# Kernel optimization log

Hardware: AMD Instinct MI355X
Metric: run time of the kernel (lower is better)

Reference implementation:

```python
import jax, jax.numpy as jnp
import numpy as np

B, D = 4096, 128
TEMPERATURE = 0.2

def setup_inputs() -> dict:
    key = jax.random.key(0)
    k1, k2 = jax.random.split(key)
    z1 = jax.random.normal(k1, (B, D), dtype=jnp.float32)
    z2 = jax.random.normal(k2, (B, D), dtype=jnp.float32)
    return {"z1": z1, "z2": z2}

def reference(z1, z2):
    # single-process path: global batch == local batch
    gb = z1.shape[0]
    z = jnp.concatenate([z1, z2], axis=0)              # [2B, D]
    sim = jnp.matmul(z, z.T) / TEMPERATURE             # [2B, 2B]
    n = 2 * gb
    diag = jnp.eye(n, dtype=bool)
    sim = jnp.where(diag, jnp.finfo(sim.dtype).min, sim)
    targets = jnp.concatenate([jnp.arange(gb, n), jnp.arange(0, gb)])
    logp = jax.nn.log_softmax(sim, axis=-1)            # [2B, 2B]
    loss_all = -logp[jnp.arange(n), targets]           # [2B]
    # rank 0, world_size 1 -> idx_keep covers all rows
    return loss_all.mean()
```

## Files before the change

kernel.cpp:

```cpp
#include <hip/hip_runtime.h>
#include <stdint.h>

typedef unsigned short u16;
typedef unsigned int u32;

#define NTOT 8192
#define BH   4096
#define DD   128
#define COLSPLIT 8
#define COLS_PER_SPLIT (NTOT / COLSPLIT)
#define TILE_COLS 128
#define TILES_PER_SPLIT (COLS_PER_SPLIT / TILE_COLS)
#define ROWS_PER_BLOCK 128
#define ROWS_PER_WAVE 32
#define LDS_PITCH 136
#define NEG_INF (-3.0e38f)
#define SCALE_IN 2.68579144f
#define LN2F 0.6931471805599453f

typedef __bf16 bf16x8 __attribute__((ext_vector_type(8)));
typedef float  f32x4  __attribute__((ext_vector_type(4)));

__device__ __forceinline__ u16 f2bf(float f) {
  u32 u = __float_as_uint(f);
  return (u16)((u + 0x7fffu + ((u >> 16) & 1u)) >> 16);
}

__device__ __forceinline__ float fexp2(float x) {
#if __has_builtin(__builtin_amdgcn_exp2f)
  return __builtin_amdgcn_exp2f(x);
#else
  float r; asm("v_exp_f32 %0, %1" : "=v"(r) : "v"(x)); return r;
#endif
}

__global__ __launch_bounds__(256) void ntx_convert(
    const float* __restrict__ z1, const float* __restrict__ z2,
    u16* __restrict__ zb, float* __restrict__ out) {
  if (blockIdx.x == 0 && threadIdx.x == 0) out[0] = 0.f;
  const int i = (blockIdx.x * 256 + threadIdx.x) * 4;
  const int half = BH * DD;
  float4 v = (i < half) ? *reinterpret_cast<const float4*>(z1 + i)
                        : *reinterpret_cast<const float4*>(z2 + (i - half));
  u32 lo = (u32)f2bf(v.x * SCALE_IN) | ((u32)f2bf(v.y * SCALE_IN) << 16);
  u32 hi = (u32)f2bf(v.z * SCALE_IN) | ((u32)f2bf(v.w * SCALE_IN) << 16);
  uint2 o; o.x = lo; o.y = hi;
  *reinterpret_cast<uint2*>(zb + i) = o;
}

__global__ __launch_bounds__(256, 2) void ntx_main(
    const u16* __restrict__ zb,
    float* __restrict__ m_part, float* __restrict__ l_part,
    float* __restrict__ st_part) {
  __shared__ u16 lds_tile[TILE_COLS * LDS_PITCH];

  const int tid  = threadIdx.x;
  const int wave = tid >> 6;
  const int lane = tid & 63;
  const int l15  = lane & 15;
  const int q    = lane >> 4;

  const int rwave = blockIdx.x * ROWS_PER_BLOCK + wave * ROWS_PER_WAVE;
  const int split = blockIdx.y;
  const int col0  = split * COLS_PER_SPLIT;

  bf16x8 afrag[2][4];
#pragma unroll
  for (int rt = 0; rt < 2; ++rt)
#pragma unroll
    for (int kk = 0; kk < 4; ++kk) {
      const int r = rwave + rt * 16 + l15;
      afrag[rt][kk] = *reinterpret_cast<const bf16x8*>(zb + r * DD + kk * 32 + q * 8);
    }

  float m_run[2][4], l_run[2][4], stv[2][4];
#pragma unroll
  for (int rt = 0; rt < 2; ++rt)
#pragma unroll
    for (int r = 0; r < 4; ++r) { m_run[rt][r] = NEG_INF; l_run[rt][r] = 0.f; stv[rt][r] = NEG_INF; }

  for (int t = 0; t < TILES_PER_SPLIT; ++t) {
    const int ct0 = col0 + t * TILE_COLS;

    __syncthreads();
    {
      const uint4* src = reinterpret_cast<const uint4*>(zb + ct0 * DD);
#pragma unroll
      for (int i = 0; i < 8; ++i) {
        const int c   = tid + i * 256;
        const int col = c >> 4, w16 = c & 15;
        uint4 v = src[c];
        *reinterpret_cast<uint4*>(lds_tile + col * LDS_PITCH + w16 * 8) = v;
      }
    }
    __syncthreads();

    f32x4 acc[2][8];
#pragma unroll
    for (int rt = 0; rt < 2; ++rt)
#pragma unroll
      for (int cs = 0; cs < 8; ++cs) acc[rt][cs] = (f32x4){0.f, 0.f, 0.f, 0.f};

#pragma unroll
    for (int cs = 0; cs < 8; ++cs) {
      bf16x8 bfrag[4];
#pragma unroll
      for (int kk = 0; kk < 4; ++kk)
        bfrag[kk] = *reinterpret_cast<const bf16x8*>(
            lds_tile + (cs * 16 + l15) * LDS_PITCH + kk * 32 + q * 8);
#pragma unroll
      for (int rt = 0; rt < 2; ++rt)
#pragma unroll
        for (int kk = 0; kk < 4; ++kk)
          acc[rt][cs] = __builtin_amdgcn_mfma_f32_16x16x32_bf16(
              afrag[rt][kk], bfrag[kk], acc[rt][cs], 0, 0, 0);
    }

    const bool has_diag = (rwave >= ct0) && (rwave < ct0 + TILE_COLS);
    const int  trow     = rwave ^ BH;
    const bool has_tgt  = (trow >= ct0) && (trow < ct0 + TILE_COLS);
    if (has_diag || has_tgt) {
#pragma unroll
      for (int rt = 0; rt < 2; ++rt)
#pragma unroll
        for (int r = 0; r < 4; ++r) {
          const int grow = rwave + rt * 16 + q * 4 + r;
#pragma unroll
          for (int cs = 0; cs < 8; ++cs) {
            const int gcol = ct0 + cs * 16 + l15;
            float v = acc[rt][cs][r];
            if (gcol == (grow ^ BH)) stv[rt][r] = fmaxf(stv[rt][r], v);
            if (gcol == grow) acc[rt][cs][r] = NEG_INF;
          }
        }
    }

#pragma unroll
    for (int rt = 0; rt < 2; ++rt)
#pragma unroll
      for (int r = 0; r < 4; ++r) {
        float mx = acc[rt][0][r];
#pragma unroll
        for (int cs = 1; cs < 8; ++cs) mx = fmaxf(mx, acc[rt][cs][r]);
        const float mnew = fmaxf(m_run[rt][r], mx);
        float s = 0.f;
#pragma unroll
        for (int cs = 0; cs < 8; ++cs) s += fexp2(acc[rt][cs][r] - mnew);
        l_run[rt][r] = l_run[rt][r] * fexp2(m_run[rt][r] - mnew) + s;
        m_run[rt][r] = mnew;
      }
  }

#pragma unroll
  for (int rt = 0; rt < 2; ++rt)
#pragma unroll
    for (int r = 0; r < 4; ++r) {
      float m = m_run[rt][r], l = l_run[rt][r];
#pragma unroll
      for (int off = 1; off < 16; off <<= 1) {
        const float mo = __shfl_xor(m, off, 64);
        const float lo = __shfl_xor(l, off, 64);
        const float mn = fmaxf(m, mo);
        l = l * fexp2(m - mn) + lo * fexp2(mo - mn);
        m = mn;
      }
      float sv = stv[rt][r];
#pragma unroll
      for (int off = 1; off < 16; off <<= 1) sv = fmaxf(sv, __shfl_xor(sv, off, 64));
      if (l15 == 0) {
        const int grow = rwave + rt * 16 + q * 4 + r;
        m_part[split * NTOT + grow] = m;
        l_part[split * NTOT + grow] = l;
        const int tcol = grow ^ BH;
        if (tcol >= col0 && tcol < col0 + COLS_PER_SPLIT) st_part[grow] = sv;
      }
    }
}

__global__ __launch_bounds__(256) void ntx_finish(
    const float* __restrict__ m_part, const float* __restrict__ l_part,
    const float* __restrict__ st_part, float* __restrict__ out) {
  const int row = blockIdx.x * 256 + threadIdx.x;
  float m = NEG_INF;
#pragma unroll
  for (int s = 0; s < COLSPLIT; ++s) m = fmaxf(m, m_part[s * NTOT + row]);
  float l = 0.f;
#pragma unroll
  for (int s = 0; s < COLSPLIT; ++s) l += l_part[s * NTOT + row] * fexp2(m_part[s * NTOT + row] - m);
  float loss = LN2F * (m + __log2f(l) - st_part[row]);

#pragma unroll
  for (int off = 32; off >= 1; off >>= 1) loss += __shfl_xor(loss, off, 64);
  __shared__ float wsum[4];
  if ((threadIdx.x & 63) == 0) wsum[threadIdx.x >> 6] = loss;
  __syncthreads();
  if (threadIdx.x == 0) {
    float s = wsum[0] + wsum[1] + wsum[2] + wsum[3];
    atomicAdd(out, s * (1.0f / NTOT));
  }
}

extern "C" void kernel_launch(void* const* d_in, const int* in_sizes, int n_in,
                              void* d_out, int out_size, void* d_ws, size_t ws_size,
                              hipStream_t stream) {
  const float* z1 = (const float*)d_in[0];
  const float* z2 = (const float*)d_in[1];
  float* out = (float*)d_out;

  char* ws = (char*)d_ws;
  u16*   zb      = (u16*)ws;
  float* m_part  = (float*)(ws + (size_t)NTOT * DD * 2);
  float* l_part  = m_part + COLSPLIT * NTOT;
  float* st_part = l_part + COLSPLIT * NTOT;

  ntx_convert<<<dim3((NTOT * DD) / (256 * 4)), dim3(256), 0, stream>>>(z1, z2, zb, out);
  ntx_main<<<dim3(NTOT / ROWS_PER_BLOCK, COLSPLIT), dim3(256), 0, stream>>>(
      zb, m_part, l_part, st_part);
  ntx_finish<<<dim3(NTOT / 256), dim3(256), 0, stream>>>(m_part, l_part, st_part, out);
}
```

Measured before the change: 87.39 us.

## Prefetch next column tile into registers and shrink tiles for more occupancy

Adds register staging so the global load of the next column tile overlaps the MFMA and softmax work on the current tile, with the LDS write moved after compute. The tile width is halved to 64 columns and the column split doubled to 16, which gives a larger grid, and the occupancy hint is raised to 3 blocks per CU. In exchange the kernel does more online-softmax rescale steps per row, writes twice as many partial results for the finish pass to combine, and has less register headroom under the tighter launch bound.

```diff
diff --git a/kernel.cpp b/kernel.cpp
--- a/kernel.cpp
+++ b/kernel.cpp
@@ -7,9 +7,9 @@
 #define NTOT 8192
 #define BH   4096
 #define DD   128
-#define COLSPLIT 8
+#define COLSPLIT 16
 #define COLS_PER_SPLIT (NTOT / COLSPLIT)
-#define TILE_COLS 128
+#define TILE_COLS 64
 #define TILES_PER_SPLIT (COLS_PER_SPLIT / TILE_COLS)
 #define ROWS_PER_BLOCK 128
 #define ROWS_PER_WAVE 32
@@ -48,7 +48,7 @@
   *reinterpret_cast<uint2*>(zb + i) = o;
 }
 
-__global__ __launch_bounds__(256, 2) void ntx_main(
+__global__ __launch_bounds__(256, 3) void ntx_main(
     const u16* __restrict__ zb,
     float* __restrict__ m_part, float* __restrict__ l_part,
     float* __restrict__ st_part) {
@@ -79,30 +79,40 @@
 #pragma unroll
     for (int r = 0; r < 4; ++r) { m_run[rt][r] = NEG_INF; l_run[rt][r] = 0.f; stv[rt][r] = NEG_INF; }
 
+  uint4 stg[4];
+  {
+    const uint4* s = reinterpret_cast<const uint4*>(zb + col0 * DD);
+#pragma unroll
+    for (int j = 0; j < 4; ++j) stg[j] = s[tid + j * 256];
+  }
+  {
+#pragma unroll
+    for (int j = 0; j < 4; ++j) {
+      const int u = tid + j * 256;
+      const int col = u >> 4, w16 = u & 15;
+      *reinterpret_cast<uint4*>(lds_tile + col * LDS_PITCH + w16 * 8) = stg[j];
+    }
+  }
+  __syncthreads();
+
   for (int t = 0; t < TILES_PER_SPLIT; ++t) {
     const int ct0 = col0 + t * TILE_COLS;
-
-    __syncthreads();
-    {
-      const uint4* src = reinterpret_cast<const uint4*>(zb + ct0 * DD);
-#pragma unroll
-      for (int i = 0; i < 8; ++i) {
-        const int c   = tid + i * 256;
-        const int col = c >> 4, w16 = c & 15;
-        uint4 v = src[c];
-        *reinterpret_cast<uint4*>(lds_tile + col * LDS_PITCH + w16 * 8) = v;
-      }
-    }
-    __syncthreads();
-
-    f32x4 acc[2][8];
+    const bool more = (t + 1 < TILES_PER_SPLIT);
+
+    if (more) {
+      const uint4* s = reinterpret_cast<const uint4*>(zb + (ct0 + TILE_COLS) * DD);
+#pragma unroll
+      for (int j = 0; j < 4; ++j) stg[j] = s[tid + j * 256];
+    }
+
+    f32x4 acc[2][4];
 #pragma unroll
     for (int rt = 0; rt < 2; ++rt)
 #pragma unroll
-      for (int cs = 0; cs < 8; ++cs) acc[rt][cs] = (f32x4){0.f, 0.f, 0.f, 0.f};
-
-#pragma unroll
-    for (int cs = 0; cs < 8; ++cs) {
+      for (int cs = 0; cs < 4; ++cs) acc[rt][cs] = (f32x4){0.f, 0.f, 0.f, 0.f};
+
+#pragma unroll
+    for (int cs = 0; cs < 4; ++cs) {
       bf16x8 bfrag[4];
 #pragma unroll
       for (int kk = 0; kk < 4; ++kk)
@@ -126,7 +136,7 @@
         for (int r = 0; r < 4; ++r) {
           const int grow = rwave + rt * 16 + q * 4 + r;
 #pragma unroll
-          for (int cs = 0; cs < 8; ++cs) {
+          for (int cs = 0; cs < 4; ++cs) {
             const int gcol = ct0 + cs * 16 + l15;
             float v = acc[rt][cs][r];
             if (gcol == (grow ^ BH)) stv[rt][r] = fmaxf(stv[rt][r], v);
@@ -141,14 +151,25 @@
       for (int r = 0; r < 4; ++r) {
         float mx = acc[rt][0][r];
 #pragma unroll
-        for (int cs = 1; cs < 8; ++cs) mx = fmaxf(mx, acc[rt][cs][r]);
+        for (int cs = 1; cs < 4; ++cs) mx = fmaxf(mx, acc[rt][cs][r]);
         const float mnew = fmaxf(m_run[rt][r], mx);
         float s = 0.f;
 #pragma unroll
-        for (int cs = 0; cs < 8; ++cs) s += fexp2(acc[rt][cs][r] - mnew);
+        for (int cs = 0; cs < 4; ++cs) s += fexp2(acc[rt][cs][r] - mnew);
         l_run[rt][r] = l_run[rt][r] * fexp2(m_run[rt][r] - mnew) + s;
         m_run[rt][r] = mnew;
       }
+
+    if (more) {
+      __syncthreads();
+#pragma unroll
+      for (int j = 0; j < 4; ++j) {
+        const int u = tid + j * 256;
+        const int col = u >> 4, w16 = u & 15;
+        *reinterpret_cast<uint4*>(lds_tile + col * LDS_PITCH + w16 * 8) = stg[j];
+      }
+      __syncthreads();
+    }
   }
 
 #pragma unroll
```

Result: slower. 105.7 us (+20.9%).
